# Kernel tuning notes

Hardware: AMD Instinct MI355X
Metric: run time of the kernel (lower is better)

Reference implementation:

```python
import jax, jax.numpy as jnp
import numpy as np

C = 512  # channels

def _maxpool2x2(x):
    # x: [B,H,W,C] -> [B,H/2,W/2,C]
    B, H, W, Cc = x.shape
    return x.reshape(B, H // 2, 2, W // 2, 2, Cc).max(axis=(2, 4))

def setup_inputs() -> dict:
    key = jax.random.key(0)
    ks = jax.random.split(key, 6)
    x = jax.random.normal(ks[0], (16, 64, 64, C), dtype=jnp.float32)
    # 1x1 conv kernels stored as [C_in, C_out]; spectral norm treated as identity
    # on the (already-normalized) effective weights.
    s = lambda k, i, o: jax.random.normal(k, (i, o), dtype=jnp.float32) / np.sqrt(i)
    W_theta = s(ks[1], C, C // 8)
    W_phi = s(ks[2], C, C // 8)
    W_g = s(ks[3], C, C // 2)
    W_o = s(ks[4], C // 2, C)
    gamma = jnp.float32(0.7)  # nonzero so the attention path matters
    return {"x": x, "W_theta": W_theta, "W_phi": W_phi, "W_g": W_g,
            "W_o": W_o, "gamma": gamma}

def reference(x, W_theta, W_phi, W_g, W_o, gamma):
    B, H, W, Cc = x.shape
    S = H * W            # query length
    Sk = S // 4          # key/value length after 2x2 maxpool
    theta = jnp.einsum('bhwc,cd->bhwd', x, W_theta)              # [B,H,W,C/8]
    phi = _maxpool2x2(jnp.einsum('bhwc,cd->bhwd', x, W_phi))     # [B,H/2,W/2,C/8]
    g = _maxpool2x2(jnp.einsum('bhwc,cd->bhwd', x, W_g))         # [B,H/2,W/2,C/2]
    theta = theta.reshape(B, S, Cc // 8)
    phi = phi.reshape(B, Sk, Cc // 8)
    g = g.reshape(B, Sk, Cc // 2)
    # scores [B,S,Sk]; SAGAN omits the 1/sqrt(d_k) scaling
    beta = jax.nn.softmax(jnp.einsum('bqd,bkd->bqk', theta, phi), axis=-1)
    tmp = jnp.einsum('bqk,bkv->bqv', beta, g).reshape(B, H, W, Cc // 2)
    o = jnp.einsum('bhwv,vc->bhwc', tmp, W_o)
    return gamma * o + x
```

## Files before the change

kernel.cpp:

```cpp
#include <hip/hip_runtime.h>

typedef __attribute__((ext_vector_type(8))) short bf16x8;
typedef __attribute__((ext_vector_type(4))) float f32x4;
typedef unsigned short u16;
typedef unsigned int u32;

#define MFMA __builtin_amdgcn_mfma_f32_16x16x32_bf16

static __device__ __forceinline__ float b2f(u16 u) {
    u32 x = ((u32)u) << 16;
    return __builtin_bit_cast(float, x);
}
static __device__ __forceinline__ u16 f2b(float f) {
    u32 u = __builtin_bit_cast(u32, f);
    u32 r = (u + 0x7fffu + ((u >> 16) & 1u)) >> 16;
    return (u16)r;
}
static __device__ __forceinline__ void async16(const u16* g, u16* l) {
    __builtin_amdgcn_global_load_lds(
        (const __attribute__((address_space(1))) u32*)g,
        (__attribute__((address_space(3))) u32*)l, 16, 0, 0);
}

__global__ __launch_bounds__(256) void xcast(const float* __restrict__ x, u16* __restrict__ xb) {
    size_t i = ((size_t)blockIdx.x * 256 + threadIdx.x) * 8;
    f32x4 f0 = *(const f32x4*)(x + i);
    f32x4 f1 = *(const f32x4*)(x + i + 4);
    bf16x8 v;
    v[0] = (short)f2b(f0[0]); v[1] = (short)f2b(f0[1]);
    v[2] = (short)f2b(f0[2]); v[3] = (short)f2b(f0[3]);
    v[4] = (short)f2b(f1[0]); v[5] = (short)f2b(f1[1]);
    v[6] = (short)f2b(f1[2]); v[7] = (short)f2b(f1[3]);
    *(bf16x8*)(xb + i) = v;
}

__global__ void pack_w(const float* __restrict__ Wt, const float* __restrict__ Wp,
                       const float* __restrict__ Wg, const float* __restrict__ Wo,
                       u16* __restrict__ WcatT, u16* __restrict__ WoT) {
    int t = blockIdx.x * 256 + threadIdx.x;
    const int n1 = 384 * 512;
    if (t < n1) {
        int n = t >> 9, k = t & 511;
        float v;
        if (n < 64)       v = Wt[k * 64 + n];
        else if (n < 128) v = Wp[k * 64 + (n - 64)];
        else              v = Wg[k * 256 + (n - 128)];
        WcatT[t] = f2b(v);
    } else {
        int j = t - n1;
        if (j < 512 * 256) {
            int n = j >> 8, k = j & 255;
            WoT[j] = f2b(Wo[k * 512 + n]);
        }
    }
}

template <int K>
static __device__ __forceinline__ void gemm_core(const u16* __restrict__ A,
                                                 const u16* __restrict__ Bt,
                                                 int m0, int n0, int lda, int ldb,
                                                 f32x4 acc[4][4], u16* As, u16* Bs) {
    const int t = threadIdx.x;
    const int w = t >> 6, li = t & 15, quad = (t >> 4) & 3;
    const int wm = (w & 1) << 6, wn = (w >> 1) << 6;
#pragma unroll
    for (int mi = 0; mi < 4; mi++)
#pragma unroll
        for (int ni = 0; ni < 4; ni++) acc[mi][ni] = (f32x4)0.0f;
    const u16* ag = A + (size_t)(m0 + (t >> 2)) * lda + ((t & 3) << 3);
    const u16* bg = Bt + (size_t)(n0 + (t >> 2)) * ldb + ((t & 3) << 3);
    u16* asw = As + w * 512;
    u16* bsw = Bs + w * 512;
    for (int k0 = 0; k0 < K; k0 += 32) {
        __syncthreads();
        async16(ag + k0, asw);
        async16(ag + k0 + (size_t)64 * lda, asw + 2048);
        async16(bg + k0, bsw);
        async16(bg + k0 + (size_t)64 * ldb, bsw + 2048);
        __syncthreads();
        bf16x8 af[4], bfr[4];
#pragma unroll
        for (int mi = 0; mi < 4; mi++)
            af[mi] = *(const bf16x8*)(As + (wm + mi * 16 + li) * 32 + quad * 8);
#pragma unroll
        for (int ni = 0; ni < 4; ni++)
            bfr[ni] = *(const bf16x8*)(Bs + (wn + ni * 16 + li) * 32 + quad * 8);
#pragma unroll
        for (int mi = 0; mi < 4; mi++)
#pragma unroll
            for (int ni = 0; ni < 4; ni++)
                acc[mi][ni] = MFMA(af[mi], bfr[ni], acc[mi][ni], 0, 0, 0);
    }
    __syncthreads();
}

static __device__ __forceinline__ void epi_bf16(const f32x4 acc[4][4], u16* ebuf,
                                                u16* __restrict__ outp, int ld,
                                                int row0, int col0) {
    const int t = threadIdx.x;
    const int li = t & 15, quad = (t >> 4) & 3;
#pragma unroll
    for (int mi = 0; mi < 4; mi++)
#pragma unroll
        for (int ni = 0; ni < 4; ni++)
#pragma unroll
            for (int r = 0; r < 4; r++)
                ebuf[(mi * 16 + quad * 4 + r) * 72 + ni * 16 + li] = f2b(acc[mi][ni][r]);
    const int rr = (t & 63) >> 3, cc = (t & 7) * 8;
#pragma unroll
    for (int j = 0; j < 8; j++) {
        int row = j * 8 + rr;
        bf16x8 v = *(const bf16x8*)(ebuf + row * 72 + cc);
        *(bf16x8*)(outp + (size_t)(row0 + row) * ld + col0 + cc) = v;
    }
}

__global__ __launch_bounds__(256) void proj_gemm(const u16* __restrict__ xb,
                                                 const u16* __restrict__ WcatT,
                                                 u16* __restrict__ theta,
                                                 u16* __restrict__ ppg) {
    __shared__ __attribute__((aligned(16))) u16 sbuf[18432];
    u16* As = sbuf;
    u16* Bs = sbuf + 4096;
    int bm = blockIdx.x / 3, bn = blockIdx.x % 3;
    f32x4 acc[4][4];
    gemm_core<512>(xb, WcatT, bm * 128, bn * 128, 512, 512, acc, As, Bs);
    const int w = threadIdx.x >> 6;
    u16* ebuf = sbuf + w * 4608;
    int row0 = bm * 128 + (w & 1) * 64;
    int gcol = bn * 128 + (w >> 1) * 64;
    if (gcol < 64) epi_bf16(acc, ebuf, theta, 64, row0, 0);
    else           epi_bf16(acc, ebuf, ppg, 320, row0, gcol - 64);
}

__global__ void pool_phi(const u16* __restrict__ ppg, u16* __restrict__ phi) {
    int t = blockIdx.x * 256 + threadIdx.x;
    int c = t & 63;
    int pos = (t >> 6) & 1023;
    int b = t >> 16;
    int h2 = pos >> 5, w2 = pos & 31;
    size_t base = ((size_t)(b << 12) + h2 * 128 + w2 * 2) * 320 + c;
    float v0 = b2f(ppg[base]), v1 = b2f(ppg[base + 320]);
    float v2 = b2f(ppg[base + 320 * 64]), v3 = b2f(ppg[base + 320 * 65]);
    float m = fmaxf(fmaxf(v0, v1), fmaxf(v2, v3));
    phi[((size_t)(b << 10) + pos) * 64 + c] = f2b(m);
}

__global__ void pool_gt(const u16* __restrict__ ppg, u16* __restrict__ gT) {
    __shared__ float tile[64][65];
    int bid = blockIdx.x;
    int b = bid >> 6;
    int rem = bid & 63;
    int c0 = (rem >> 4) * 64;
    int pos0 = (rem & 15) * 64;
    int t = threadIdx.x;
#pragma unroll
    for (int i = 0; i < 16; i++) {
        int o = t + i * 256;
        int cl = o & 63, pl = o >> 6;
        int pos = pos0 + pl;
        int h2 = pos >> 5, w2 = pos & 31;
        size_t base = ((size_t)(b << 12) + h2 * 128 + w2 * 2) * 320 + 64 + c0 + cl;
        float v0 = b2f(ppg[base]), v1 = b2f(ppg[base + 320]);
        float v2 = b2f(ppg[base + 320 * 64]), v3 = b2f(ppg[base + 320 * 65]);
        tile[pl][cl] = fmaxf(fmaxf(v0, v1), fmaxf(v2, v3));
    }
    __syncthreads();
    int cl = t >> 2, ch = t & 3;
    u16 valbuf[16] __attribute__((aligned(16)));
#pragma unroll
    for (int j = 0; j < 16; j++) valbuf[j] = f2b(tile[ch * 16 + j][cl]);
    u16* dst = gT + ((size_t)b * 256 + c0 + cl) * 1024 + pos0 + ch * 16;
    *(uint4*)(dst) = *(const uint4*)(valbuf);
    *(uint4*)(dst + 8) = *(const uint4*)(valbuf + 8);
}

__global__ __launch_bounds__(256, 2) void attn_fused(const u16* __restrict__ theta,
                                                     const u16* __restrict__ phi,
                                                     const u16* __restrict__ gT,
                                                     u16* __restrict__ tmp) {
    __shared__ __attribute__((aligned(16))) u16 lds[28672];
    u16* stgP = lds;
    u16* stgG = lds + 4096;
    u16* pbuf = lds + 20480;

    int bid = blockIdx.x;
    int swz = (bid & 7) * 64 + (bid >> 3);
    int b = swz >> 5;
    int q0 = (swz & 31) << 7;
    const int t = threadIdx.x;
    const int w = t >> 6, li = t & 15, quad = (t >> 4) & 3;

    const u16* thp = theta + (((size_t)(b << 12) + q0 + w * 32 + li) << 6) + quad * 8;
    bf16x8 tq[2][2];
    tq[0][0] = *(const bf16x8*)thp;
    tq[0][1] = *(const bf16x8*)(thp + 32);
    tq[1][0] = *(const bf16x8*)(thp + (16 << 6));
    tq[1][1] = *(const bf16x8*)(thp + (16 << 6) + 32);

    const int srow = t >> 3;
    const int sc = (t & 7) ^ (srow & 7);
    const u16* phisrc = phi + ((size_t)(b << 10) + srow) * 64 + sc * 8;
    const u16* gsrc = gT + ((size_t)(b << 8) + srow) * 1024 + sc * 8;
    u16* pbq[2] = {pbuf + (w * 2 + 0) * 1024, pbuf + (w * 2 + 1) * 1024};

    f32x4 o[2][16];
#pragma unroll
    for (int qg = 0; qg < 2; qg++)
#pragma unroll
        for (int ni = 0; ni < 16; ni++) o[qg][ni] = (f32x4)0.0f;
    float m[2] = {-3.0e38f, -3.0e38f}, sum[2] = {0.0f, 0.0f};

    for (int kc = 0; kc < 16; kc++) {
        __syncthreads();
        async16(phisrc + (size_t)(kc * 64) * 64, stgP + w * 512);
        async16(phisrc + (size_t)(kc * 64 + 32) * 64, stgP + 2048 + w * 512);
#pragma unroll
        for (int j = 0; j < 8; j++)
            async16(gsrc + (size_t)(j * 32) * 1024 + kc * 64, stgG + j * 2048 + w * 512);
        __syncthreads();

        f32x4 sacc[2][4];
#pragma unroll
        for (int qg = 0; qg < 2; qg++)
#pragma unroll
            for (int nf = 0; nf < 4; nf++) sacc[qg][nf] = (f32x4)0.0f;
#pragma unroll
        for (int nf = 0; nf < 4; nf++) {
            int row = nf * 16 + li;
            int p0 = quad ^ (li & 7);
            int p1 = (4 + quad) ^ (li & 7);
            bf16x8 f0 = *(const bf16x8*)(stgP + row * 64 + p0 * 8);
            bf16x8 f1 = *(const bf16x8*)(stgP + row * 64 + p1 * 8);
            sacc[0][nf] = MFMA(f0, tq[0][0], sacc[0][nf], 0, 0, 0);
            sacc[0][nf] = MFMA(f1, tq[0][1], sacc[0][nf], 0, 0, 0);
            sacc[1][nf] = MFMA(f0, tq[1][0], sacc[1][nf], 0, 0, 0);
            sacc[1][nf] = MFMA(f1, tq[1][1], sacc[1][nf], 0, 0, 0);
        }

#pragma unroll
        for (int qg = 0; qg < 2; qg++) {
            float mc = sacc[qg][0][0];
#pragma unroll
            for (int nf = 0; nf < 4; nf++)
#pragma unroll
                for (int r = 0; r < 4; r++) mc = fmaxf(mc, sacc[qg][nf][r]);
            mc = fmaxf(mc, __shfl_xor(mc, 16, 64));
            mc = fmaxf(mc, __shfl_xor(mc, 32, 64));
            if (!__all(mc <= m[qg] + 8.0f)) {
                float nm = fmaxf(m[qg], mc);
                float f = __expf(m[qg] - nm);
                sum[qg] *= f;
#pragma unroll
                for (int ni = 0; ni < 16; ni++)
#pragma unroll
                    for (int r = 0; r < 4; r++) o[qg][ni][r] *= f;
                m[qg] = nm;
            }
            float p[16];
            float s = 0.0f;
#pragma unroll
            for (int nf = 0; nf < 4; nf++)
#pragma unroll
                for (int r = 0; r < 4; r++) {
                    float e = __expf(sacc[qg][nf][r] - m[qg]);
                    p[nf * 4 + r] = e;
                    s += e;
                }
            s += __shfl_xor(s, 16, 64);
            s += __shfl_xor(s, 32, 64);
            sum[qg] += s;

            u16* pb = pbq[qg];
#pragma unroll
            for (int nf = 0; nf < 4; nf++) {
                int cc = nf * 2 + (quad >> 1);
                int pos = cc ^ (li & 7);
                u32* dst = (u32*)(pb + li * 64 + pos * 8 + (quad & 1) * 4);
                dst[0] = (u32)f2b(p[nf * 4 + 0]) | ((u32)f2b(p[nf * 4 + 1]) << 16);
                dst[1] = (u32)f2b(p[nf * 4 + 2]) | ((u32)f2b(p[nf * 4 + 3]) << 16);
            }
        }

#pragma unroll
        for (int w2 = 0; w2 < 2; w2++) {
            int pos8 = ((w2 * 4 + quad) ^ (li & 7)) * 8;
            bf16x8 pf0 = *(const bf16x8*)(pbq[0] + li * 64 + pos8);
            bf16x8 pf1 = *(const bf16x8*)(pbq[1] + li * 64 + pos8);
#pragma unroll
            for (int ni = 0; ni < 16; ni++) {
                bf16x8 gf = *(const bf16x8*)(stgG + (ni * 16 + li) * 64 + pos8);
                o[0][ni] = MFMA(gf, pf0, o[0][ni], 0, 0, 0);
                o[1][ni] = MFMA(gf, pf1, o[1][ni], 0, 0, 0);
            }
        }
    }

    float inv[2] = {1.0f / sum[0], 1.0f / sum[1]};
#pragma unroll
    for (int qg = 0; qg < 2; qg++)
#pragma unroll
        for (int ni = 0; ni < 16; ni++)
#pragma unroll
            for (int r = 0; r < 4; r++) o[qg][ni][r] *= inv[qg];

    __syncthreads();
    u16* eb = lds + w * 4224;
    const int lane = t & 63;
#pragma unroll
    for (int qg = 0; qg < 2; qg++) {
#pragma unroll
        for (int ni = 0; ni < 16; ni++) {
            u32* d = (u32*)(eb + li * 264 + ni * 16 + quad * 4);
            d[0] = (u32)f2b(o[qg][ni][0]) | ((u32)f2b(o[qg][ni][1]) << 16);
            d[1] = (u32)f2b(o[qg][ni][2]) | ((u32)f2b(o[qg][ni][3]) << 16);
        }
#pragma unroll
        for (int pss = 0; pss < 8; pss++) {
            int row = pss * 2 + (lane >> 5);
            bf16x8 v = *(const bf16x8*)(eb + row * 264 + (lane & 31) * 8);
            *(bf16x8*)(tmp + ((size_t)(b << 12) + q0 + w * 32 + qg * 16 + row) * 256 +
                       (lane & 31) * 8) = v;
        }
    }
}

__global__ __launch_bounds__(256) void out_gemm(const u16* __restrict__ tmp,
                                                const u16* __restrict__ WoT,
                                                const float* __restrict__ x,
                                                const float* __restrict__ gamma_p,
                                                float* __restrict__ out) {
    __shared__ __attribute__((aligned(16))) u16 sbuf[18432];
    u16* As = sbuf;
    u16* Bs = sbuf + 4096;
    int bm = blockIdx.x >> 2, bn = blockIdx.x & 3;
    f32x4 acc[4][4];
    gemm_core<256>(tmp, WoT, bm * 128, bn * 128, 256, 256, acc, As, Bs);
    float gamma = gamma_p[0];
    const int t = threadIdx.x;
    const int w = t >> 6, li = t & 15, quad = (t >> 4) & 3;
    int row0 = bm * 128 + (w & 1) * 64;
    int col0 = bn * 128 + (w >> 1) * 64;
    float* fb = (float*)sbuf + w * 2176;
    const int rr = (t & 63) >> 4, ccv = (t & 15) * 4;
#pragma unroll
    for (int half = 0; half < 2; half++) {
#pragma unroll
        for (int mi = 0; mi < 2; mi++)
#pragma unroll
            for (int ni = 0; ni < 4; ni++)
#pragma unroll
                for (int r = 0; r < 4; r++)
                    fb[(mi * 16 + quad * 4 + r) * 68 + ni * 16 + li] =
                        acc[half * 2 + mi][ni][r];
#pragma unroll
        for (int j = 0; j < 8; j++) {
            int row = j * 4 + rr;
            f32x4 v = *(const f32x4*)(fb + row * 68 + ccv);
            size_t go = (size_t)(row0 + half * 32 + row) * 512 + col0 + ccv;
            f32x4 xv = *(const f32x4*)(x + go);
#pragma unroll
            for (int e = 0; e < 4; e++) v[e] = gamma * v[e] + xv[e];
            *(f32x4*)(out + go) = v;
        }
    }
}

extern "C" void kernel_launch(void* const* d_in, const int* in_sizes, int n_in,
                              void* d_out, int out_size, void* d_ws, size_t ws_size,
                              hipStream_t stream) {
    (void)in_sizes; (void)n_in; (void)out_size; (void)ws_size;
    const float* x  = (const float*)d_in[0];
    const float* Wt = (const float*)d_in[1];
    const float* Wp = (const float*)d_in[2];
    const float* Wg = (const float*)d_in[3];
    const float* Wo = (const float*)d_in[4];
    const float* gm = (const float*)d_in[5];
    float* out = (float*)d_out;

    char* ws = (char*)d_ws;
    size_t off = 0;
    u16* WcatT = (u16*)(ws + off); off += (size_t)384 * 512 * 2;
    u16* WoT   = (u16*)(ws + off); off += (size_t)512 * 256 * 2;
    u16* xb    = (u16*)(ws + off); off += (size_t)65536 * 512 * 2;
    u16* theta = (u16*)(ws + off); off += (size_t)65536 * 64 * 2;
    u16* ppg   = (u16*)(ws + off); off += (size_t)65536 * 320 * 2;
    u16* phi = xb;
    u16* gT  = xb + (size_t)16 * 1024 * 64;
    u16* tmp = ppg;

    pack_w<<<1280, 256, 0, stream>>>(Wt, Wp, Wg, Wo, WcatT, WoT);
    xcast<<<16384, 256, 0, stream>>>(x, xb);
    proj_gemm<<<1536, 256, 0, stream>>>(xb, WcatT, theta, ppg);
    pool_phi<<<4096, 256, 0, stream>>>(ppg, phi);
    pool_gt<<<1024, 256, 0, stream>>>(ppg, gT);
    attn_fused<<<512, 256, 0, stream>>>(theta, phi, gT, tmp);
    out_gemm<<<2048, 256, 0, stream>>>(tmp, WoT, x, gm, out);
}
```

Measured before the change: 410.5 us.

## Double-buffer GEMM LDS tiles, swizzle block order, shrink epilogue LDS

The shared GEMM core now prefetches the next K-slice into a second LDS buffer while the MFMAs consume the current one, cutting the two barriers per iteration down to one. The projection and output GEMMs remap block IDs across 8 groups, likely to spread work across XCDs and improve L2 locality. Both epilogues are split into smaller chunks so they fit in the reduced 32KB LDS, and the output epilogue issues the residual x loads before the LDS transpose. Issuing the next global_load_lds before the MFMAs of the current buffer relies on the single barrier per step for correctness, and the extra buffer raises register and LDS pressure.

```diff
diff --git a/kernel.cpp b/kernel.cpp
--- a/kernel.cpp
+++ b/kernel.cpp
@@ -59,7 +59,7 @@
 static __device__ __forceinline__ void gemm_core(const u16* __restrict__ A,
                                                  const u16* __restrict__ Bt,
                                                  int m0, int n0, int lda, int ldb,
-                                                 f32x4 acc[4][4], u16* As, u16* Bs) {
+                                                 f32x4 acc[4][4], u16* S) {
     const int t = threadIdx.x;
     const int w = t >> 6, li = t & 15, quad = (t >> 4) & 3;
     const int wm = (w & 1) << 6, wn = (w >> 1) << 6;
@@ -69,15 +69,24 @@
         for (int ni = 0; ni < 4; ni++) acc[mi][ni] = (f32x4)0.0f;
     const u16* ag = A + (size_t)(m0 + (t >> 2)) * lda + ((t & 3) << 3);
     const u16* bg = Bt + (size_t)(n0 + (t >> 2)) * ldb + ((t & 3) << 3);
-    u16* asw = As + w * 512;
-    u16* bsw = Bs + w * 512;
+    const int ws = w * 512;
+    async16(ag, S + ws);
+    async16(ag + (size_t)64 * lda, S + ws + 2048);
+    async16(bg, S + 4096 + ws);
+    async16(bg + (size_t)64 * ldb, S + 4096 + ws + 2048);
+    __syncthreads();
+    int cur = 0;
+#pragma unroll
     for (int k0 = 0; k0 < K; k0 += 32) {
-        __syncthreads();
-        async16(ag + k0, asw);
-        async16(ag + k0 + (size_t)64 * lda, asw + 2048);
-        async16(bg + k0, bsw);
-        async16(bg + k0 + (size_t)64 * ldb, bsw + 2048);
-        __syncthreads();
+        if (k0 + 32 < K) {
+            u16* nS = S + (cur ^ 1) * 8192;
+            async16(ag + k0 + 32, nS + ws);
+            async16(ag + k0 + 32 + (size_t)64 * lda, nS + ws + 2048);
+            async16(bg + k0 + 32, nS + 4096 + ws);
+            async16(bg + k0 + 32 + (size_t)64 * ldb, nS + 4096 + ws + 2048);
+        }
+        const u16* As = S + cur * 8192;
+        const u16* Bs = As + 4096;
         bf16x8 af[4], bfr[4];
 #pragma unroll
         for (int mi = 0; mi < 4; mi++)
@@ -90,8 +99,9 @@
 #pragma unroll
             for (int ni = 0; ni < 4; ni++)
                 acc[mi][ni] = MFMA(af[mi], bfr[ni], acc[mi][ni], 0, 0, 0);
-    }
-    __syncthreads();
+        __syncthreads();
+        cur ^= 1;
+    }
 }
 
 static __device__ __forceinline__ void epi_bf16(const f32x4 acc[4][4], u16* ebuf,
@@ -99,19 +109,23 @@
                                                 int row0, int col0) {
     const int t = threadIdx.x;
     const int li = t & 15, quad = (t >> 4) & 3;
-#pragma unroll
-    for (int mi = 0; mi < 4; mi++)
-#pragma unroll
-        for (int ni = 0; ni < 4; ni++)
-#pragma unroll
-            for (int r = 0; r < 4; r++)
-                ebuf[(mi * 16 + quad * 4 + r) * 72 + ni * 16 + li] = f2b(acc[mi][ni][r]);
     const int rr = (t & 63) >> 3, cc = (t & 7) * 8;
 #pragma unroll
-    for (int j = 0; j < 8; j++) {
-        int row = j * 8 + rr;
-        bf16x8 v = *(const bf16x8*)(ebuf + row * 72 + cc);
-        *(bf16x8*)(outp + (size_t)(row0 + row) * ld + col0 + cc) = v;
+    for (int h = 0; h < 2; h++) {
+#pragma unroll
+        for (int m2 = 0; m2 < 2; m2++)
+#pragma unroll
+            for (int ni = 0; ni < 4; ni++)
+#pragma unroll
+                for (int r = 0; r < 4; r++)
+                    ebuf[(m2 * 16 + quad * 4 + r) * 72 + ni * 16 + li] =
+                        f2b(acc[h * 2 + m2][ni][r]);
+#pragma unroll
+        for (int j = 0; j < 4; j++) {
+            int row = j * 8 + rr;
+            bf16x8 v = *(const bf16x8*)(ebuf + row * 72 + cc);
+            *(bf16x8*)(outp + (size_t)(row0 + h * 32 + row) * ld + col0 + cc) = v;
+        }
     }
 }
 
@@ -119,14 +133,14 @@
                                                  const u16* __restrict__ WcatT,
                                                  u16* __restrict__ theta,
                                                  u16* __restrict__ ppg) {
-    __shared__ __attribute__((aligned(16))) u16 sbuf[18432];
-    u16* As = sbuf;
-    u16* Bs = sbuf + 4096;
-    int bm = blockIdx.x / 3, bn = blockIdx.x % 3;
+    __shared__ __attribute__((aligned(16))) u16 sbuf[16384];
+    int bid = blockIdx.x;
+    int sbid = (bid & 7) * 192 + (bid >> 3);
+    int bm = sbid / 3, bn = sbid % 3;
     f32x4 acc[4][4];
-    gemm_core<512>(xb, WcatT, bm * 128, bn * 128, 512, 512, acc, As, Bs);
+    gemm_core<512>(xb, WcatT, bm * 128, bn * 128, 512, 512, acc, sbuf);
     const int w = threadIdx.x >> 6;
-    u16* ebuf = sbuf + w * 4608;
+    u16* ebuf = sbuf + w * 2304;
     int row0 = bm * 128 + (w & 1) * 64;
     int gcol = bn * 128 + (w >> 1) * 64;
     if (gcol < 64) epi_bf16(acc, ebuf, theta, 64, row0, 0);
@@ -330,37 +344,39 @@
                                                 const float* __restrict__ x,
                                                 const float* __restrict__ gamma_p,
                                                 float* __restrict__ out) {
-    __shared__ __attribute__((aligned(16))) u16 sbuf[18432];
-    u16* As = sbuf;
-    u16* Bs = sbuf + 4096;
-    int bm = blockIdx.x >> 2, bn = blockIdx.x & 3;
+    __shared__ __attribute__((aligned(16))) u16 sbuf[16384];
+    int bid = blockIdx.x;
+    int sbid = (bid & 7) * 256 + (bid >> 3);
+    int bm = sbid >> 2, bn = sbid & 3;
     f32x4 acc[4][4];
-    gemm_core<256>(tmp, WoT, bm * 128, bn * 128, 256, 256, acc, As, Bs);
+    gemm_core<256>(tmp, WoT, bm * 128, bn * 128, 256, 256, acc, sbuf);
     float gamma = gamma_p[0];
     const int t = threadIdx.x;
     const int w = t >> 6, li = t & 15, quad = (t >> 4) & 3;
     int row0 = bm * 128 + (w & 1) * 64;
     int col0 = bn * 128 + (w >> 1) * 64;
-    float* fb = (float*)sbuf + w * 2176;
-    const int rr = (t & 63) >> 4, ccv = (t & 15) * 4;
-#pragma unroll
-    for (int half = 0; half < 2; half++) {
-#pragma unroll
-        for (int mi = 0; mi < 2; mi++)
-#pragma unroll
-            for (int ni = 0; ni < 4; ni++)
-#pragma unroll
-                for (int r = 0; r < 4; r++)
-                    fb[(mi * 16 + quad * 4 + r) * 68 + ni * 16 + li] =
-                        acc[half * 2 + mi][ni][r];
-#pragma unroll
-        for (int j = 0; j < 8; j++) {
-            int row = j * 4 + rr;
-            f32x4 v = *(const f32x4*)(fb + row * 68 + ccv);
-            size_t go = (size_t)(row0 + half * 32 + row) * 512 + col0 + ccv;
-            f32x4 xv = *(const f32x4*)(x + go);
-#pragma unroll
-            for (int e = 0; e < 4; e++) v[e] = gamma * v[e] + xv[e];
+    float* fb = (float*)sbuf + w * 1088;
+    const int lane = t & 63;
+    const int rhi = lane >> 4, cl = (lane & 15) * 4;
+#pragma unroll
+    for (int mi = 0; mi < 4; mi++) {
+        f32x4 xv[4];
+#pragma unroll
+        for (int j = 0; j < 4; j++) {
+            size_t go = (size_t)(row0 + mi * 16 + j * 4 + rhi) * 512 + col0 + cl;
+            xv[j] = *(const f32x4*)(x + go);
+        }
+#pragma unroll
+        for (int ni = 0; ni < 4; ni++)
+#pragma unroll
+            for (int r = 0; r < 4; r++)
+                fb[(quad * 4 + r) * 68 + ni * 16 + li] = acc[mi][ni][r];
+#pragma unroll
+        for (int j = 0; j < 4; j++) {
+            f32x4 v = *(const f32x4*)(fb + (j * 4 + rhi) * 68 + cl);
+#pragma unroll
+            for (int e = 0; e < 4; e++) v[e] = gamma * v[e] + xv[j][e];
+            size_t go = (size_t)(row0 + mi * 16 + j * 4 + rhi) * 512 + col0 + cl;
             *(f32x4*)(out + go) = v;
         }
     }
```

Measured after the change: 389.7 us. 1.05x faster.
